# Kernel tuning notes

Hardware: AMD Instinct MI355X
Metric: run time of the kernel (lower is better)

The kernel has to match this reference:

```python
import jax, jax.numpy as jnp
import numpy as np

N_NODES = 100000


def _gcn_conv(x, W, b, row, col, norm, n):
    # PyG GCNConv: h = x @ W, then symmetric-normalized scatter-add, then bias
    h = x @ W                          # [N, out]
    msg = h[col] * norm[:, None]       # gather at source nodes, scale per-edge
    out = jax.ops.segment_sum(msg, row, num_segments=n)  # scatter-add to dest
    return out + b


def setup_inputs() -> dict:
    key = jax.random.key(0)
    k1, k2, k3, k4, k5, k6 = jax.random.split(key, 6)
    F_in, H, C = 128, 128, 64
    E = 1600000
    x = jax.random.normal(k1, (N_NODES, F_in), dtype=jnp.float32)
    edge_index = jax.random.randint(k2, (2, E), 0, N_NODES, dtype=jnp.int64)
    s1 = 1.0 / np.sqrt(F_in)
    s2 = 1.0 / np.sqrt(H)
    W1 = jax.random.uniform(k3, (F_in, H), jnp.float32, -s1, s1)
    b1 = jax.random.uniform(k4, (H,), jnp.float32, -s1, s1)
    W2 = jax.random.uniform(k5, (H, C), jnp.float32, -s2, s2)
    b2 = jax.random.uniform(k6, (C,), jnp.float32, -s2, s2)
    return {"x": x, "edge_index": edge_index, "W1": W1, "b1": b1, "W2": W2, "b2": b2}


def reference(x, edge_index, W1, b1, W2, b2):
    n = x.shape[0]
    # add self-loops (GCNConv default)
    loops = jnp.arange(n, dtype=edge_index.dtype)
    row = jnp.concatenate([edge_index[0], loops])  # destination
    col = jnp.concatenate([edge_index[1], loops])  # source
    # symmetric normalization deg^{-1/2}[row] * deg^{-1/2}[col]
    deg = jax.ops.segment_sum(jnp.ones_like(row, dtype=x.dtype), row, num_segments=n)
    dinv = jnp.where(deg > 0, jax.lax.rsqrt(deg), 0.0)
    norm = dinv[row] * dinv[col]       # [E+N]
    h = jax.nn.relu(_gcn_conv(x, W1, b1, row, col, norm, n))
    # dropout is identity in eval mode
    out = _gcn_conv(h, W2, b2, row, col, norm, n)
    return jax.nn.log_softmax(out, axis=1)
```

## Files before the change

### kernel.cpp

```cpp
#include <hip/hip_runtime.h>
#include <hip/hip_fp16.h>
#include <cstdint>
#include <cstddef>

#define TPB 256
#define NWIN 8
#define CAP 64

using half8 = __attribute__((ext_vector_type(8))) _Float16;
using f32x4 = __attribute__((ext_vector_type(4))) float;

__global__ void k_setup(const void* __restrict__ ei, int E, int N,
                        const float* __restrict__ W1, const float* __restrict__ W2,
                        _Float16* __restrict__ wf1, _Float16* __restrict__ wf2,
                        int* __restrict__ cnt, int2* __restrict__ pairs, int nCnt) {
    int b = blockIdx.x;
    if (b < 16) {
        int i = b * TPB + threadIdx.x;
        int k  = i >> 5;
        int n0 = (i & 31) * 4;
        float4 w = ((const float4*)W1)[i];
        int ct = n0 >> 4, kb = k >> 5;
        int lane0 = ((k >> 3) & 3) * 16 + (n0 & 15);
        int j = k & 7;
        int base = ((ct * 4 + kb) * 64 + lane0) * 8 + j;
        wf1[base]      = (_Float16)w.x;
        wf1[base + 8]  = (_Float16)w.y;
        wf1[base + 16] = (_Float16)w.z;
        wf1[base + 24] = (_Float16)w.w;
    } else if (b < 24) {
        int i = (b - 16) * TPB + threadIdx.x;
        int k  = i >> 4;
        int n0 = (i & 15) * 4;
        float4 w = ((const float4*)W2)[i];
        int ct = n0 >> 4, kb = k >> 5;
        int lane0 = ((k >> 3) & 3) * 16 + (n0 & 15);
        int j = k & 7;
        int base = ((ct * 4 + kb) * 64 + lane0) * 8 + j;
        wf2[base]      = (_Float16)w.x;
        wf2[base + 8]  = (_Float16)w.y;
        wf2[base + 16] = (_Float16)w.z;
        wf2[base + 24] = (_Float16)w.w;
    } else if (b < 24 + nCnt) {
        int i = (b - 24) * TPB + threadIdx.x;
        if (i < N) cnt[i] = 0;
    } else {
        __shared__ int bad;
        if (threadIdx.x == 0) bad = 0;
        __syncthreads();
        if (threadIdx.x < 256) {
            long long v = ((const long long*)ei)[threadIdx.x];
            if (v < 0 || v >= (long long)N) bad = 1;
        }
        __syncthreads();
        int is64 = !bad;
        int base = ((b - 24 - nCnt) * TPB + threadIdx.x) * 4;
        if (base >= E) return;
        if (is64) {
            const long long* e64 = (const long long*)ei;
#pragma unroll
            for (int k = 0; k < 4; ++k)
                if (base + k < E)
                    pairs[base + k] = make_int2((int)e64[base + k],
                                                (int)e64[(long long)E + base + k]);
        } else {
            const int* e32 = (const int*)ei;
#pragma unroll
            for (int k = 0; k < 4; ++k)
                if (base + k < E)
                    pairs[base + k] = make_int2(e32[base + k], e32[E + base + k]);
        }
    }
}

__global__ __launch_bounds__(256)
void k_mega(const int2* __restrict__ pairs, int E, int winRows, int N,
            int* __restrict__ cnt, int* __restrict__ slots,
            const float* __restrict__ x, const half8* __restrict__ wf1,
            __half* __restrict__ xw1, int nFill, int nGemm) {
    __shared__ __align__(16) _Float16 Of[4][16 * 136];

    if ((int)blockIdx.x < nFill) {
        const int w = blockIdx.x & (NWIN - 1);
        const int lo = w * winRows, hi = lo + winRows;
        const int nChunks = (E + 1023) >> 10;
        const int stride = nFill / NWIN;
        for (int chunk = blockIdx.x / NWIN; chunk < nChunks; chunk += stride) {
            int base = (chunk << 10) + threadIdx.x * 4;
            if (base >= E) continue;
            int2 p[4];
            if (base + 3 < E) {
                const int4* p4 = (const int4*)(pairs + base);
                int4 u0 = p4[0], u1 = p4[1];
                p[0] = make_int2(u0.x, u0.y); p[1] = make_int2(u0.z, u0.w);
                p[2] = make_int2(u1.x, u1.y); p[3] = make_int2(u1.z, u1.w);
            } else {
#pragma unroll
                for (int k = 0; k < 4; ++k)
                    p[k] = (base + k < E) ? pairs[base + k] : make_int2(-1, -1);
            }
            int pos[4];
#pragma unroll
            for (int k = 0; k < 4; ++k) {
                bool in = (p[k].x >= lo && p[k].x < hi);
                pos[k] = in ? atomicAdd(&cnt[p[k].x], 1) : -1;
            }
#pragma unroll
            for (int k = 0; k < 4; ++k)
                if (pos[k] >= 0 && pos[k] < CAP)
                    slots[(size_t)p[k].x * CAP + pos[k]] = p[k].y;
        }
    } else {
        const int gb = blockIdx.x - nFill;
        const int wave = threadIdx.x >> 6, lane = threadIdx.x & 63;
        const int m = lane & 15, quad = lane >> 4;
        const int nRowTiles = (N + 15) >> 4;

        for (int rt = gb * 4 + wave; rt < nRowTiles; rt += nGemm * 4) {
            const int row0 = rt * 16;
            const int arow = row0 + m;
            const bool rvalid = arow < N;
            const float* xrow = x + (size_t)(rvalid ? arow : 0) * 128;

            f32x4 acc[8];
#pragma unroll
            for (int ct = 0; ct < 8; ++ct) acc[ct] = (f32x4){0.f, 0.f, 0.f, 0.f};

#pragma unroll
            for (int kb = 0; kb < 4; ++kb) {
                const float4* ap = (const float4*)(xrow + kb * 32 + quad * 8);
                float4 a0 = ap[0], a1 = ap[1];
                half8 a;
                a[0] = (_Float16)a0.x; a[1] = (_Float16)a0.y;
                a[2] = (_Float16)a0.z; a[3] = (_Float16)a0.w;
                a[4] = (_Float16)a1.x; a[5] = (_Float16)a1.y;
                a[6] = (_Float16)a1.z; a[7] = (_Float16)a1.w;
#pragma unroll
                for (int ct = 0; ct < 8; ++ct) {
                    half8 b = wf1[(ct * 4 + kb) * 64 + lane];
                    acc[ct] = __builtin_amdgcn_mfma_f32_16x16x32_f16(a, b, acc[ct], 0, 0, 0);
                }
            }

            _Float16* myO = &Of[wave][0];
#pragma unroll
            for (int ct = 0; ct < 8; ++ct)
#pragma unroll
                for (int r = 0; r < 4; ++r)
                    myO[(quad * 4 + r) * 136 + ct * 16 + m] = (_Float16)acc[ct][r];
            int vr = N - row0; if (vr > 16) vr = 16;
            float4* dst = (float4*)(xw1 + (size_t)row0 * 128);
            for (int i = lane; i < vr * 16; i += 64) {
                int r = i >> 4, q = i & 15;
                dst[r * 16 + q] = *(const float4*)&myO[r * 136 + q * 8];
            }
        }
    }
}

__global__ __launch_bounds__(256)
void k_g1g2(const __half* __restrict__ xw1, const int* __restrict__ cnt,
            const int* __restrict__ slots, const float* __restrict__ bias,
            const half8* __restrict__ wf2, __half* __restrict__ xw2, int N) {
    __shared__ __align__(16) _Float16 Ht[16 * 136];
    __shared__ __align__(16) _Float16 Of[16 * 72];

    const int row0 = blockIdx.x * 16;
    const int local = threadIdx.x >> 4;
    const int lane16 = threadIdx.x & 15;
    const int node = row0 + local;

    {
        union { __half2 h2[4]; float4 f; } u;
        if (node < N) {
            int cn = cnt[node];
            int len = cn > CAP ? CAP : cn;
            float dvn = rsqrtf((float)cn + 1.0f);
            const int* sl = slots + (size_t)node * CAP;
            float acc[8];
            {
                float4 raw = *(const float4*)(xw1 + (size_t)node * 128 + lane16 * 8);
                const __half2* hp = (const __half2*)&raw;
#pragma unroll
                for (int k = 0; k < 4; ++k) {
                    float2 f = __half22float2(hp[k]);
                    acc[2 * k] = dvn * f.x; acc[2 * k + 1] = dvn * f.y;
                }
            }
            int j = 0;
            for (; j + 3 < len; j += 4) {
                int4 cc = *(const int4*)(sl + j);
                float dv0 = rsqrtf((float)cnt[cc.x] + 1.0f);
                float dv1 = rsqrtf((float)cnt[cc.y] + 1.0f);
                float dv2 = rsqrtf((float)cnt[cc.z] + 1.0f);
                float dv3 = rsqrtf((float)cnt[cc.w] + 1.0f);
                float4 raw0 = *(const float4*)(xw1 + (size_t)cc.x * 128 + lane16 * 8);
                float4 raw1 = *(const float4*)(xw1 + (size_t)cc.y * 128 + lane16 * 8);
                float4 raw2 = *(const float4*)(xw1 + (size_t)cc.z * 128 + lane16 * 8);
                float4 raw3 = *(const float4*)(xw1 + (size_t)cc.w * 128 + lane16 * 8);
                const __half2* h0 = (const __half2*)&raw0;
                const __half2* h1 = (const __half2*)&raw1;
                const __half2* h2 = (const __half2*)&raw2;
                const __half2* h3 = (const __half2*)&raw3;
#pragma unroll
                for (int k = 0; k < 4; ++k) {
                    float2 f0 = __half22float2(h0[k]);
                    float2 f1 = __half22float2(h1[k]);
                    float2 f2 = __half22float2(h2[k]);
                    float2 f3 = __half22float2(h3[k]);
                    acc[2 * k]     = fmaf(dv0, f0.x, fmaf(dv1, f1.x,
                                     fmaf(dv2, f2.x, fmaf(dv3, f3.x, acc[2 * k]))));
                    acc[2 * k + 1] = fmaf(dv0, f0.y, fmaf(dv1, f1.y,
                                     fmaf(dv2, f2.y, fmaf(dv3, f3.y, acc[2 * k + 1]))));
                }
            }
            for (; j < len; ++j) {
                int c = sl[j];
                float dv = rsqrtf((float)cnt[c] + 1.0f);
                float4 raw = *(const float4*)(xw1 + (size_t)c * 128 + lane16 * 8);
                const __half2* hp = (const __half2*)&raw;
#pragma unroll
                for (int k = 0; k < 4; ++k) {
                    float2 f = __half22float2(hp[k]);
                    acc[2 * k]     = fmaf(dv, f.x, acc[2 * k]);
                    acc[2 * k + 1] = fmaf(dv, f.y, acc[2 * k + 1]);
                }
            }
            float4 b01 = ((const float4*)bias)[lane16 * 2];
            float4 b23 = ((const float4*)bias)[lane16 * 2 + 1];
            float v[8];
            v[0] = b01.x + dvn * acc[0]; v[1] = b01.y + dvn * acc[1];
            v[2] = b01.z + dvn * acc[2]; v[3] = b01.w + dvn * acc[3];
            v[4] = b23.x + dvn * acc[4]; v[5] = b23.y + dvn * acc[5];
            v[6] = b23.z + dvn * acc[6]; v[7] = b23.w + dvn * acc[7];
#pragma unroll
            for (int k = 0; k < 4; ++k)
                u.h2[k] = __floats2half2_rn(fmaxf(v[2 * k], 0.f), fmaxf(v[2 * k + 1], 0.f));
        } else {
            u.f = make_float4(0.f, 0.f, 0.f, 0.f);
        }
        *(float4*)(Ht + local * 136 + lane16 * 8) = u.f;
    }
    __syncthreads();

    {
        const int wave = threadIdx.x >> 6, lane = threadIdx.x & 63;
        const int m = lane & 15, quad = lane >> 4;
        f32x4 acc = (f32x4){0.f, 0.f, 0.f, 0.f};
#pragma unroll
        for (int kb = 0; kb < 4; ++kb) {
            half8 a = *(const half8*)(Ht + m * 136 + kb * 32 + quad * 8);
            half8 b = wf2[(wave * 4 + kb) * 64 + lane];
            acc = __builtin_amdgcn_mfma_f32_16x16x32_f16(a, b, acc, 0, 0, 0);
        }
#pragma unroll
        for (int r = 0; r < 4; ++r)
            Of[(quad * 4 + r) * 72 + wave * 16 + m] = (_Float16)acc[r];
    }
    __syncthreads();
    {
        int vr = N - row0; if (vr > 16) vr = 16;
        float4* dst = (float4*)(xw2 + (size_t)row0 * 64);
        for (int i = threadIdx.x; i < vr * 8; i += TPB) {
            int r = i >> 3, q = i & 7;
            dst[r * 8 + q] = *(const float4*)&Of[r * 72 + q * 8];
        }
    }
}

__global__ void k_gather2_lsm(const __half* __restrict__ xws, const int* __restrict__ cnt,
                              const int* __restrict__ slots,
                              const float* __restrict__ bias, float* __restrict__ out, int N) {
    long long t = (long long)blockIdx.x * TPB + threadIdx.x;
    int node = (int)(t >> 4);
    int lane = (int)(t & 15);
    if (node >= N) return;
    int cn = cnt[node];
    int len = cn > CAP ? CAP : cn;
    float dvn = rsqrtf((float)cn + 1.0f);
    const int* sl = slots + (size_t)node * CAP;
    float a0, a1, a2, a3;
    {
        float2 raw = *(const float2*)(xws + (size_t)node * 64 + lane * 4);
        const __half2* hp = (const __half2*)&raw;
        float2 f0 = __half22float2(hp[0]), f1 = __half22float2(hp[1]);
        a0 = dvn * f0.x; a1 = dvn * f0.y; a2 = dvn * f1.x; a3 = dvn * f1.y;
    }
    int j = 0;
    for (; j + 3 < len; j += 4) {
        int4 cc = *(const int4*)(sl + j);
        float dv0 = rsqrtf((float)cnt[cc.x] + 1.0f);
        float dv1 = rsqrtf((float)cnt[cc.y] + 1.0f);
        float dv2 = rsqrtf((float)cnt[cc.z] + 1.0f);
        float dv3 = rsqrtf((float)cnt[cc.w] + 1.0f);
        float2 raw0 = *(const float2*)(xws + (size_t)cc.x * 64 + lane * 4);
        float2 raw1 = *(const float2*)(xws + (size_t)cc.y * 64 + lane * 4);
        float2 raw2 = *(const float2*)(xws + (size_t)cc.z * 64 + lane * 4);
        float2 raw3 = *(const float2*)(xws + (size_t)cc.w * 64 + lane * 4);
        const __half2* h0 = (const __half2*)&raw0;
        const __half2* h1 = (const __half2*)&raw1;
        const __half2* h2 = (const __half2*)&raw2;
        const __half2* h3 = (const __half2*)&raw3;
        float2 f00 = __half22float2(h0[0]), f01 = __half22float2(h0[1]);
        float2 f10 = __half22float2(h1[0]), f11 = __half22float2(h1[1]);
        float2 f20 = __half22float2(h2[0]), f21 = __half22float2(h2[1]);
        float2 f30 = __half22float2(h3[0]), f31 = __half22float2(h3[1]);
        a0 = fmaf(dv0, f00.x, fmaf(dv1, f10.x, fmaf(dv2, f20.x, fmaf(dv3, f30.x, a0))));
        a1 = fmaf(dv0, f00.y, fmaf(dv1, f10.y, fmaf(dv2, f20.y, fmaf(dv3, f30.y, a1))));
        a2 = fmaf(dv0, f01.x, fmaf(dv1, f11.x, fmaf(dv2, f21.x, fmaf(dv3, f31.x, a2))));
        a3 = fmaf(dv0, f01.y, fmaf(dv1, f11.y, fmaf(dv2, f21.y, fmaf(dv3, f31.y, a3))));
    }
    for (; j < len; ++j) {
        int c = sl[j];
        float dv = rsqrtf((float)cnt[c] + 1.0f);
        float2 raw = *(const float2*)(xws + (size_t)c * 64 + lane * 4);
        const __half2* hp = (const __half2*)&raw;
        float2 f0 = __half22float2(hp[0]), f1 = __half22float2(hp[1]);
        a0 = fmaf(dv, f0.x, a0); a1 = fmaf(dv, f0.y, a1);
        a2 = fmaf(dv, f1.x, a2); a3 = fmaf(dv, f1.y, a3);
    }
    float4 bb = ((const float4*)bias)[lane];
    float v0 = bb.x + dvn * a0, v1 = bb.y + dvn * a1;
    float v2 = bb.z + dvn * a2, v3 = bb.w + dvn * a3;

    float m = fmaxf(fmaxf(v0, v1), fmaxf(v2, v3));
#pragma unroll
    for (int off = 1; off < 16; off <<= 1) m = fmaxf(m, __shfl_xor(m, off));
    float s = expf(v0 - m) + expf(v1 - m) + expf(v2 - m) + expf(v3 - m);
#pragma unroll
    for (int off = 1; off < 16; off <<= 1) s += __shfl_xor(s, off);
    float ls = m + logf(s);
    ((float4*)(out + (size_t)node * 64))[lane] =
        make_float4(v0 - ls, v1 - ls, v2 - ls, v3 - ls);
}

extern "C" void kernel_launch(void* const* d_in, const int* in_sizes, int n_in,
                              void* d_out, int out_size, void* d_ws, size_t ws_size,
                              hipStream_t stream) {
    const float* x  = (const float*)d_in[0];
    const void*  ei = d_in[1];
    const float* W1 = (const float*)d_in[2];
    const float* b1 = (const float*)d_in[3];
    const float* W2 = (const float*)d_in[4];
    const float* b2 = (const float*)d_in[5];
    float* out = (float*)d_out;

    const int N = in_sizes[0] / 128;
    const int E = in_sizes[1] / 2;

    char* base = (char*)d_ws;
    size_t off = 0;
    auto alloc = [&](size_t bytes) { char* p = base + off; off = (off + bytes + 255) & ~(size_t)255; return p; };
    int*      cnt   = (int*)alloc((size_t)N * sizeof(int));
    _Float16* wf1   = (_Float16*)alloc(128 * 128 * sizeof(_Float16));
    _Float16* wf2   = (_Float16*)alloc(128 * 64 * sizeof(_Float16));
    int2*     pairs = (int2*)alloc((size_t)E * sizeof(int2));
    int*      slots = (int*)alloc((size_t)N * CAP * sizeof(int));
    __half*   xw1   = (__half*)alloc((size_t)N * 128 * sizeof(__half));
    __half*   xw2   = (__half*)alloc((size_t)N * 64 * sizeof(__half));
    (void)ws_size;

    const int winRows = (N + NWIN - 1) / NWIN;
    const int nFill = 1024, nGemm = 512;
    const int nodeTiles = (N + 15) / 16;
    const int nCnt = (N + TPB - 1) / TPB;
    const int nDec = (E + TPB * 4 - 1) / (TPB * 4);

    k_setup<<<24 + nCnt + nDec, TPB, 0, stream>>>(ei, E, N, W1, W2, wf1, wf2,
                                                  cnt, pairs, nCnt);

    k_mega<<<nFill + nGemm, TPB, 0, stream>>>(pairs, E, winRows, N, cnt, slots,
                                              x, (const half8*)wf1, xw1, nFill, nGemm);

    k_g1g2<<<nodeTiles, TPB, 0, stream>>>(xw1, cnt, slots, b1, (const half8*)wf2, xw2, N);

    {
        long long t = (long long)N * 16;
        k_gather2_lsm<<<(int)((t + TPB - 1) / TPB), TPB, 0, stream>>>(xw2, cnt, slots, b2, out, N);
    }
}
```

Before: 290.2 us.

## Prescale layer-2 features by source degree and interleave fill/GEMM blocks

The layer-2 projected features are now multiplied by each node's deg^-1/2 when k_g1g2 writes them out. The final gather can then sum neighbor rows directly, without loading cnt and computing rsqrt for every edge. Separately, k_mega now interleaves slot-fill blocks and GEMM blocks in a 2:1 pattern across the grid instead of putting one kind first, so both kinds of work run concurrently across CUs. Prescaling rounds to fp16 after the multiply, which slightly changes numerics, and the interleaved mapping assumes nFill and nGemm match the 2:1 group split.

```diff
diff --git a/kernel.cpp b/kernel.cpp
--- a/kernel.cpp
+++ b/kernel.cpp
@@ -80,12 +80,16 @@
             __half* __restrict__ xw1, int nFill, int nGemm) {
     __shared__ __align__(16) _Float16 Of[4][16 * 136];
 
-    if ((int)blockIdx.x < nFill) {
+    const int g  = (int)blockIdx.x >> 3;
+    const int gm = g % 3;
+
+    if (gm != 2) {
         const int w = blockIdx.x & (NWIN - 1);
         const int lo = w * winRows, hi = lo + winRows;
+        const int fgrp = (g / 3) * 2 + gm;
         const int nChunks = (E + 1023) >> 10;
         const int stride = nFill / NWIN;
-        for (int chunk = blockIdx.x / NWIN; chunk < nChunks; chunk += stride) {
+        for (int chunk = fgrp; chunk < nChunks; chunk += stride) {
             int base = (chunk << 10) + threadIdx.x * 4;
             if (base >= E) continue;
             int2 p[4];
@@ -111,7 +115,7 @@
                     slots[(size_t)p[k].x * CAP + pos[k]] = p[k].y;
         }
     } else {
-        const int gb = blockIdx.x - nFill;
+        const int gb = (g / 3) * 8 + ((int)blockIdx.x & 7);
         const int wave = threadIdx.x >> 6, lane = threadIdx.x & 63;
         const int m = lane & 15, quad = lane >> 4;
         const int nRowTiles = (N + 15) >> 4;
@@ -164,6 +168,7 @@
             const half8* __restrict__ wf2, __half* __restrict__ xw2, int N) {
     __shared__ __align__(16) _Float16 Ht[16 * 136];
     __shared__ __align__(16) _Float16 Of[16 * 72];
+    __shared__ float dv16[16];
 
     const int row0 = blockIdx.x * 16;
     const int local = threadIdx.x >> 4;
@@ -172,10 +177,11 @@
 
     {
         union { __half2 h2[4]; float4 f; } u;
+        float dvn = 0.f;
         if (node < N) {
             int cn = cnt[node];
             int len = cn > CAP ? CAP : cn;
-            float dvn = rsqrtf((float)cn + 1.0f);
+            dvn = rsqrtf((float)cn + 1.0f);
             const int* sl = slots + (size_t)node * CAP;
             float acc[8];
             {
@@ -239,6 +245,7 @@
         } else {
             u.f = make_float4(0.f, 0.f, 0.f, 0.f);
         }
+        if (lane16 == 0) dv16[local] = dvn;
         *(float4*)(Ht + local * 136 + lane16 * 8) = u.f;
     }
     __syncthreads();
@@ -255,7 +262,8 @@
         }
 #pragma unroll
         for (int r = 0; r < 4; ++r)
-            Of[(quad * 4 + r) * 72 + wave * 16 + m] = (_Float16)acc[r];
+            Of[(quad * 4 + r) * 72 + wave * 16 + m] =
+                (_Float16)(acc[r] * dv16[quad * 4 + r]);
     }
     __syncthreads();
     {
@@ -284,15 +292,11 @@
         float2 raw = *(const float2*)(xws + (size_t)node * 64 + lane * 4);
         const __half2* hp = (const __half2*)&raw;
         float2 f0 = __half22float2(hp[0]), f1 = __half22float2(hp[1]);
-        a0 = dvn * f0.x; a1 = dvn * f0.y; a2 = dvn * f1.x; a3 = dvn * f1.y;
+        a0 = f0.x; a1 = f0.y; a2 = f1.x; a3 = f1.y;
     }
     int j = 0;
     for (; j + 3 < len; j += 4) {
         int4 cc = *(const int4*)(sl + j);
-        float dv0 = rsqrtf((float)cnt[cc.x] + 1.0f);
-        float dv1 = rsqrtf((float)cnt[cc.y] + 1.0f);
-        float dv2 = rsqrtf((float)cnt[cc.z] + 1.0f);
-        float dv3 = rsqrtf((float)cnt[cc.w] + 1.0f);
         float2 raw0 = *(const float2*)(xws + (size_t)cc.x * 64 + lane * 4);
         float2 raw1 = *(const float2*)(xws + (size_t)cc.y * 64 + lane * 4);
         float2 raw2 = *(const float2*)(xws + (size_t)cc.z * 64 + lane * 4);
@@ -305,19 +309,17 @@
         float2 f10 = __half22float2(h1[0]), f11 = __half22float2(h1[1]);
         float2 f20 = __half22float2(h2[0]), f21 = __half22float2(h2[1]);
         float2 f30 = __half22float2(h3[0]), f31 = __half22float2(h3[1]);
-        a0 = fmaf(dv0, f00.x, fmaf(dv1, f10.x, fmaf(dv2, f20.x, fmaf(dv3, f30.x, a0))));
-        a1 = fmaf(dv0, f00.y, fmaf(dv1, f10.y, fmaf(dv2, f20.y, fmaf(dv3, f30.y, a1))));
-        a2 = fmaf(dv0, f01.x, fmaf(dv1, f11.x, fmaf(dv2, f21.x, fmaf(dv3, f31.x, a2))));
-        a3 = fmaf(dv0, f01.y, fmaf(dv1, f11.y, fmaf(dv2, f21.y, fmaf(dv3, f31.y, a3))));
+        a0 += (f00.x + f10.x) + (f20.x + f30.x);
+        a1 += (f00.y + f10.y) + (f20.y + f30.y);
+        a2 += (f01.x + f11.x) + (f21.x + f31.x);
+        a3 += (f01.y + f11.y) + (f21.y + f31.y);
     }
     for (; j < len; ++j) {
         int c = sl[j];
-        float dv = rsqrtf((float)cnt[c] + 1.0f);
         float2 raw = *(const float2*)(xws + (size_t)c * 64 + lane * 4);
         const __half2* hp = (const __half2*)&raw;
         float2 f0 = __half22float2(hp[0]), f1 = __half22float2(hp[1]);
-        a0 = fmaf(dv, f0.x, a0); a1 = fmaf(dv, f0.y, a1);
-        a2 = fmaf(dv, f1.x, a2); a3 = fmaf(dv, f1.y, a3);
+        a0 += f0.x; a1 += f0.y; a2 += f1.x; a3 += f1.y;
     }
     float4 bb = ((const float4*)bias)[lane];
     float v0 = bb.x + dvn * a0, v1 = bb.y + dvn * a1;
```

Measured after the change: 288.0 us. No clear change (-0.7%).
